# Optimization experiments

Hardware: AMD Instinct MI355X
Metric: run time of the kernel (lower is better)

Reference implementation:

```python
import jax, jax.numpy as jnp
import numpy as np

EPS = 1e-5  # torch LayerNorm default eps
B, N, D_IN, E, H, V = 4096, 32, 256, 128, 512, 32

def _ln(x):
    # LayerNorm without affine (elementwise_affine=False), biased variance
    m = jnp.mean(x, axis=-1, keepdims=True)
    v = jnp.mean(jnp.square(x - m), axis=-1, keepdims=True)
    return (x - m) * jax.lax.rsqrt(v + EPS)

def _ln_gru_cell(x, h, i2h_W, i2h_b, h2h_W, h2h_b, hW_W, hW_b, hU_W, hU_b):
    gates = jax.nn.sigmoid(_ln(x @ i2h_W + i2h_b) + _ln(h @ h2h_W + h2h_b))  # [B,2H]
    hs = h.shape[-1]
    z_t = gates[:, :hs]
    r_t = gates[:, hs:]
    h_hat = jnp.tanh(_ln(x @ hW_W + hW_b) + r_t * _ln(h @ hU_W + hU_b))
    return (1.0 - z_t) * h + z_t * h_hat

def setup_inputs() -> dict:
    key = jax.random.key(0)
    ks = jax.random.split(key, 32)
    std0 = 1.0 / np.sqrt(H)
    u = lambda k, shp: jax.random.uniform(k, shp, jnp.float32, -std0, std0)
    in0 = 3 * E  # attn context + msg embedding + feedback embedding
    inp = {
        'sender_messages_embedded': jax.random.normal(ks[0], (B, E), jnp.float32),
        'prev_hidden': jax.random.normal(ks[1], (2, B, H), jnp.float32),
        'candidate_objects': jax.random.normal(ks[2], (B, N, D_IN), jnp.float32),
        'prev_msg_embedding': jax.random.normal(ks[3], (B, E), jnp.float32),
        # linear_objects_in_keys
        'Wk': jax.random.normal(ks[4], (D_IN, E), jnp.float32) * 0.05,
        'bk': jnp.zeros((E,), jnp.float32),
        # LayerNormGRUCell layer 0 (input 3E)
        'i2h_W0': u(ks[5], (in0, 2 * H)), 'i2h_b0': u(ks[6], (2 * H,)),
        'h2h_W0': u(ks[7], (H, 2 * H)), 'h2h_b0': u(ks[8], (2 * H,)),
        'hW_W0': u(ks[9], (in0, H)), 'hW_b0': u(ks[10], (H,)),
        'hU_W0': u(ks[11], (H, H)), 'hU_b0': u(ks[12], (H,)),
        # LayerNormGRUCell layer 1 (input H)
        'i2h_W1': u(ks[13], (H, 2 * H)), 'i2h_b1': u(ks[14], (2 * H,)),
        'h2h_W1': u(ks[15], (H, 2 * H)), 'h2h_b1': u(ks[16], (2 * H,)),
        'hW_W1': u(ks[17], (H, H)), 'hW_b1': u(ks[18], (H,)),
        'hU_W1': u(ks[19], (H, H)), 'hU_b1': u(ks[20], (H,)),
        # hidden_to_feedback_output
        'out_W': jax.random.normal(ks[21], (H, V), jnp.float32) * 0.05,
        'out_b': jnp.zeros((V,), jnp.float32),
    }
    return inp

def reference(sender_messages_embedded, prev_hidden, candidate_objects, prev_msg_embedding,
              Wk, bk,
              i2h_W0, i2h_b0, h2h_W0, h2h_b0, hW_W0, hW_b0, hU_W0, hU_b0,
              i2h_W1, i2h_b1, h2h_W1, h2h_b1, hW_W1, hW_b1, hU_W1, hU_b1,
              out_W, out_b):
    # object attention (dot): query = msg embedding, keys = projected candidates
    keys = candidate_objects @ Wk + bk                              # [B,N,E]
    scores = jnp.einsum('be,bne->bn', sender_messages_embedded, keys)
    weights = jax.nn.softmax(scores, axis=1)                        # [B,N]
    context = jnp.einsum('bn,bne->be', weights, keys)               # [B,E]
    rnn_input = jnp.concatenate([context, sender_messages_embedded, prev_msg_embedding], axis=-1)  # [B,3E]
    h0 = _ln_gru_cell(rnn_input, prev_hidden[0], i2h_W0, i2h_b0, h2h_W0, h2h_b0, hW_W0, hW_b0, hU_W0, hU_b0)
    h1 = _ln_gru_cell(h0, prev_hidden[1], i2h_W1, i2h_b1, h2h_W1, h2h_b1, hW_W1, hW_b1, hU_W1, hU_b1)
    logits = h1 @ out_W + out_b                                     # [B,V]
    logp = jax.nn.log_softmax(logits, axis=-1)
    probs = jnp.exp(logp)
    entropy = -jnp.sum(probs * logp, axis=-1)                       # [B]
    output_token = jnp.argmax(probs, axis=-1)                       # eval-mode argmax
    output_token_logits = jnp.take_along_axis(logp, output_token[:, None], axis=1)[:, 0]
    new_hidden = jnp.stack([h0, h1])                                # [2,B,H]
    return (output_token, entropy, output_token_logits, logits, new_hidden)
```

## Files before the change

### kernel.cpp

```cpp
#include <hip/hip_runtime.h>
#include <hip/hip_bf16.h>
#include <math.h>

#define B_SZ   4096
#define NCAND  32
#define DIN    256
#define E_SZ   128
#define H_SZ   512
#define VOCAB  32
#define LN_EPS 1e-5f

typedef unsigned short u16;
typedef unsigned int   u32;
typedef __attribute__((ext_vector_type(8))) short  short8;
typedef __attribute__((ext_vector_type(4))) float  floatx4;

static __device__ __forceinline__ float sigmoidf_(float x) {
    return 1.0f / (1.0f + expf(-x));
}
static __device__ __forceinline__ u16 f2bf(float x) {
    u32 u = __float_as_uint(x);
    return (u16)((u + 0x7FFFu + ((u >> 16) & 1u)) >> 16);
}
static __device__ __forceinline__ float bfbits2f(u16 h) {
    return __uint_as_float(((u32)h) << 16);
}

typedef const __attribute__((address_space(1))) unsigned int* gas_ptr;
typedef __attribute__((address_space(3)))       unsigned int* las_ptr;
static __device__ __forceinline__ void gload_lds16(const u16* g, u16* l) {
    __builtin_amdgcn_global_load_lds((gas_ptr)(const void*)g, (las_ptr)(void*)l, 16, 0, 0);
}

static __device__ __forceinline__ void split_store8(const float* __restrict__ g,
                                                    u16* __restrict__ sh,
                                                    u16* __restrict__ sl)
{
    float4 a = *(const float4*)g;
    float4 b = *(const float4*)(g + 4);
    float v[8] = {a.x, a.y, a.z, a.w, b.x, b.y, b.z, b.w};
    union { u16 us[8]; uint4 q; } hb, lb;
    #pragma unroll
    for (int j = 0; j < 8; ++j) {
        u16 h = f2bf(v[j]);
        hb.us[j] = h;
        lb.us[j] = f2bf(v[j] - bfbits2f(h));
    }
    *(uint4*)sh = hb.q;
    *(uint4*)sl = lb.q;
}


__global__ __launch_bounds__(256)
void transpose_split_w(const float* __restrict__ W1, const float* __restrict__ W2,
                       int N1, int N2, int K,
                       u16* __restrict__ Wt_hi, u16* __restrict__ Wt_lo)
{
    __shared__ float t[64][68];
    const int n0 = blockIdx.x * 64, k0 = blockIdx.y * 64;
    const int tid = threadIdx.x;
    const int KT = K >> 5;

    {
        const int kl = tid >> 4, nl4 = (tid & 15) * 4;
        const int ng = n0 + nl4;
        const float* src; int col, ld;
        if (ng < N1) { src = W1; col = ng;      ld = N1; }
        else         { src = W2; col = ng - N1; ld = N2; }
        #pragma unroll
        for (int p = 0; p < 4; ++p) {
            float4 v = *(const float4*)(src + (size_t)(k0 + kl + p * 16) * ld + col);
            *(float4*)&t[kl + p * 16][nl4] = v;
        }
    }
    __syncthreads();

    const int nl = tid >> 2, kc = tid & 3;
    union { u16 us[16]; uint4 v[2]; } hb, lb;
    #pragma unroll
    for (int j = 0; j < 16; ++j) {
        float x = t[kc * 16 + j][nl];
        u16 h = f2bf(x);
        float r = x - bfbits2f(h);
        hb.us[j] = h;
        lb.us[j] = f2bf(r);
    }
    const int n  = n0 + nl;
    const int kb = k0 + kc * 16;
    const size_t off = ((size_t)(n >> 7) * KT + (kb >> 5)) * 4096
                     + (size_t)(n & 127) * 32 + (kb & 31);
    *(uint4*)(Wt_hi + off)     = hb.v[0];
    *(uint4*)(Wt_hi + off + 8) = hb.v[1];
    *(uint4*)(Wt_lo + off)     = lb.v[0];
    *(uint4*)(Wt_lo + off + 8) = lb.v[1];
}

__global__ __launch_bounds__(256)
void bias_cat4_kernel(const float* __restrict__ a0, const float* __restrict__ c0, float* __restrict__ o0,
                      const float* __restrict__ a1, const float* __restrict__ c1, float* __restrict__ o1,
                      const float* __restrict__ a2, const float* __restrict__ c2, float* __restrict__ o2,
                      const float* __restrict__ a3, const float* __restrict__ c3, float* __restrict__ o3)
{
    const int t = blockIdx.x * 256 + threadIdx.x;
    const int w = t / 1536;
    const int i = t - w * 1536;
    const float* a; const float* c; float* o;
    if      (w == 0) { a = a0; c = c0; o = o0; }
    else if (w == 1) { a = a1; c = c1; o = o1; }
    else if (w == 2) { a = a2; c = c2; o = o2; }
    else             { a = a3; c = c3; o = o3; }
    o[i] = (i < 1024) ? a[i] : c[i - 1024];
}

__global__ __launch_bounds__(256)
void split_blocked_kernel(const float* __restrict__ src,
                          u16* __restrict__ hi, u16* __restrict__ lo)
{
    const int i = blockIdx.x * 256 + threadIdx.x;
    const int m = i >> 6, kq = (i & 63) << 3;
    const size_t idx = ((size_t)(m >> 7) * 16 + (kq >> 5)) * 4096
                     + (size_t)(m & 127) * 32 + (kq & 31);
    split_store8(src + (size_t)m * 512 + kq, &hi[idx], &lo[idx]);
}

__global__ __launch_bounds__(256)
void mfma_gemm_dual_kernel(const u16* __restrict__ Axh, const u16* __restrict__ Axl,
                           const u16* __restrict__ Wxh, const u16* __restrict__ Wxl,
                           const float* __restrict__ bx, float* __restrict__ Cx, int KTx,
                           const u16* __restrict__ Ahh, const u16* __restrict__ Ahl,
                           const u16* __restrict__ Whh, const u16* __restrict__ Whl,
                           const float* __restrict__ bh, float* __restrict__ Ch, int KTh)
{
    __shared__ __align__(16) u16 sAh[2][4096];
    __shared__ __align__(16) u16 sAl[2][4096];
    __shared__ __align__(16) u16 sWh[2][4096];
    __shared__ __align__(16) u16 sWl[2][4096];

    const int tid  = threadIdx.x;
    const int lane = tid & 63;
    const int wave = tid >> 6;
    const int wm = (wave >> 1) * 64;
    const int wn = (wave & 1) * 64;
    const int r16 = lane & 15;
    const int q8  = (lane >> 4) * 8;

    const int f   = blockIdx.x;
    const int lin = (f & 7) * 96 + (f >> 3);
    const int sel = lin >= 384;
    const int r   = lin - (sel ? 384 : 0);
    const int mt  = r / 12;
    const int nt  = r - mt * 12;
    const int m_base = mt * 128;
    const int n_base = nt * 128;

    const u16* Ah_  = sel ? Ahh : Axh;
    const u16* Al_  = sel ? Ahl : Axl;
    const u16* Wh_  = sel ? Whh : Wxh;
    const u16* Wl_  = sel ? Whl : Wxl;
    const float* bias = sel ? bh : bx;
    float*       C    = sel ? Ch : Cx;
    const int    KT   = sel ? KTh : KTx;

    const size_t abase = (size_t)(m_base >> 7) * KT * 4096;
    const size_t wbase = (size_t)(n_base >> 7) * KT * 4096;
    const int sofs = wave * 1024;
    const int gofs = sofs + (lane << 3);

    floatx4 acc[4][4] = {};

    {
        const size_t ai = abase + gofs;
        const size_t wi = wbase + gofs;
        gload_lds16(Ah_ + ai,       &sAh[0][sofs]);
        gload_lds16(Ah_ + ai + 512, &sAh[0][sofs + 512]);
        gload_lds16(Al_ + ai,       &sAl[0][sofs]);
        gload_lds16(Al_ + ai + 512, &sAl[0][sofs + 512]);
        gload_lds16(Wh_ + wi,       &sWh[0][sofs]);
        gload_lds16(Wh_ + wi + 512, &sWh[0][sofs + 512]);
        gload_lds16(Wl_ + wi,       &sWl[0][sofs]);
        gload_lds16(Wl_ + wi + 512, &sWl[0][sofs + 512]);
    }

    int cur = 0;
    for (int kt = 0; kt < KT; ++kt) {
        __syncthreads();

        const int nxt = cur ^ 1;
        if (kt + 1 < KT) {
            const size_t ai = abase + (size_t)(kt + 1) * 4096 + gofs;
            const size_t wi = wbase + (size_t)(kt + 1) * 4096 + gofs;
            gload_lds16(Ah_ + ai,       &sAh[nxt][sofs]);
            gload_lds16(Ah_ + ai + 512, &sAh[nxt][sofs + 512]);
            gload_lds16(Al_ + ai,       &sAl[nxt][sofs]);
            gload_lds16(Al_ + ai + 512, &sAl[nxt][sofs + 512]);
            gload_lds16(Wh_ + wi,       &sWh[nxt][sofs]);
            gload_lds16(Wh_ + wi + 512, &sWh[nxt][sofs + 512]);
            gload_lds16(Wl_ + wi,       &sWl[nxt][sofs]);
            gload_lds16(Wl_ + wi + 512, &sWl[nxt][sofs + 512]);
        }

        short8 ah[4], al[4], bhf[4], blf[4];
        #pragma unroll
        for (int i = 0; i < 4; ++i) {
            const int ar = (wm + i * 16 + r16) * 32 + q8;
            ah[i] = *(const short8*)&sAh[cur][ar];
            al[i] = *(const short8*)&sAl[cur][ar];
            const int br = (wn + i * 16 + r16) * 32 + q8;
            bhf[i] = *(const short8*)&sWh[cur][br];
            blf[i] = *(const short8*)&sWl[cur][br];
        }
        #pragma unroll
        for (int i = 0; i < 4; ++i)
            #pragma unroll
            for (int j = 0; j < 4; ++j) {
                acc[i][j] = __builtin_amdgcn_mfma_f32_16x16x32_bf16(ah[i], bhf[j], acc[i][j], 0, 0, 0);
                acc[i][j] = __builtin_amdgcn_mfma_f32_16x16x32_bf16(ah[i], blf[j], acc[i][j], 0, 0, 0);
                acc[i][j] = __builtin_amdgcn_mfma_f32_16x16x32_bf16(al[i], bhf[j], acc[i][j], 0, 0, 0);
            }

        cur = nxt;
    }

    const int quad = lane >> 4;
    #pragma unroll
    for (int j = 0; j < 4; ++j) {
        const int n = n_base + wn + j * 16 + r16;
        const float bv = bias[n];
        #pragma unroll
        for (int i = 0; i < 4; ++i) {
            #pragma unroll
            for (int rr = 0; rr < 4; ++rr) {
                const int m = m_base + wm + i * 16 + quad * 4 + rr;
                C[(size_t)m * 1536 + n] = acc[i][j][rr] + bv;
            }
        }
    }
}

__global__ __launch_bounds__(256)
void gemm_bt64_kernel(const float* __restrict__ A, const float* __restrict__ Bt,
                      float* __restrict__ C, int M, int N, int K, int ldc)
{
    __shared__ float As[16][68];
    __shared__ float Bs[16][68];

    const int tid = threadIdx.x;
    const int bm = blockIdx.y * 64;
    const int bn = blockIdx.x * 64;
    const int tx = tid & 15, ty = tid >> 4;
    const int m0 = ty * 4, n0 = tx * 4;
    const int arow = tid >> 2, acol = (tid & 3) * 4;

    float acc[4][4] = {};

    for (int k0 = 0; k0 < K; k0 += 16) {
        float4 a4 = *(const float4*)(A  + (size_t)(bm + arow) * K + (k0 + acol));
        float4 b4 = *(const float4*)(Bt + (size_t)(bn + arow) * K + (k0 + acol));
        As[acol + 0][arow] = a4.x; As[acol + 1][arow] = a4.y;
        As[acol + 2][arow] = a4.z; As[acol + 3][arow] = a4.w;
        Bs[acol + 0][arow] = b4.x; Bs[acol + 1][arow] = b4.y;
        Bs[acol + 2][arow] = b4.z; Bs[acol + 3][arow] = b4.w;
        __syncthreads();
        #pragma unroll
        for (int k = 0; k < 16; ++k) {
            float4 av = *(const float4*)&As[k][m0];
            float4 bv = *(const float4*)&Bs[k][n0];
            float aa[4] = {av.x, av.y, av.z, av.w};
            float bb[4] = {bv.x, bv.y, bv.z, bv.w};
            #pragma unroll
            for (int i = 0; i < 4; ++i)
                #pragma unroll
                for (int j = 0; j < 4; ++j)
                    acc[i][j] = fmaf(aa[i], bb[j], acc[i][j]);
        }
        __syncthreads();
    }

    #pragma unroll
    for (int i = 0; i < 4; ++i)
        *(float4*)(C + (size_t)(bm + m0 + i) * ldc + bn + n0) =
            make_float4(acc[i][0], acc[i][1], acc[i][2], acc[i][3]);
}

__global__ __launch_bounds__(256)
void attn_ctx_kernel(const float* __restrict__ co, const float* __restrict__ q,
                     const float* __restrict__ snd, const float* __restrict__ pmsg,
                     float* __restrict__ cbar,
                     u16* __restrict__ rinh, u16* __restrict__ rinl)
{
    __shared__ float s_q[DIN];
    __shared__ float s_scores[NCAND];
    __shared__ float s_w[NCAND];

    const int b   = blockIdx.x;
    const int tid = threadIdx.x;
    const float* cob = co + (size_t)b * NCAND * DIN;

    if (tid < DIN) s_q[tid] = q[(size_t)b * DIN + tid];
    __syncthreads();

    {
        const int n = tid >> 3, part = tid & 7;
        const float* con = cob + n * DIN;
        float sc = 0.f;
        #pragma unroll
        for (int qq = 0; qq < 8; ++qq) {
            const int d = part * 4 + qq * 32;
            float4 cv = *(const float4*)(con + d);
            float4 qv = *(const float4*)&s_q[d];
            sc += cv.x * qv.x + cv.y * qv.y + cv.z * qv.z + cv.w * qv.w;
        }
        #pragma unroll
        for (int m = 4; m; m >>= 1) sc += __shfl_xor(sc, m);
        if (part == 0) s_scores[n] = sc;
    }
    __syncthreads();

    if (tid < NCAND) {
        float s  = s_scores[tid];
        float mx = s;
        #pragma unroll
        for (int m = 16; m; m >>= 1) mx = fmaxf(mx, __shfl_xor(mx, m));
        float e = expf(s - mx);
        float sum = e;
        #pragma unroll
        for (int m = 16; m; m >>= 1) sum += __shfl_xor(sum, m);
        s_w[tid] = e / sum;
    }
    __syncthreads();

    {
        float cb = 0.f;
        #pragma unroll
        for (int n = 0; n < NCAND; ++n) cb = fmaf(s_w[n], cob[n * DIN + tid], cb);
        cbar[(size_t)b * DIN + tid] = cb;
    }
    {
        const float x = (tid < 128) ? snd[(size_t)b * E_SZ + tid]
                                    : pmsg[(size_t)b * E_SZ + (tid - 128)];
        const int d = 128 + tid;
        const u16 h = f2bf(x);
        const u16 l = f2bf(x - bfbits2f(h));
        const size_t idx = ((size_t)(b >> 7) * 12 + (d >> 5)) * 4096
                         + (size_t)(b & 127) * 32 + (d & 31);
        rinh[idx] = h;
        rinl[idx] = l;
    }
}

__global__ __launch_bounds__(256)
void gemm_ctx_kernel(const float* __restrict__ A, const float* __restrict__ Bm,
                     const float* __restrict__ bias,
                     u16* __restrict__ rinh, u16* __restrict__ rinl)
{
    __shared__ float As[16][68];
    __shared__ float Bs[16][68];

    const int tid = threadIdx.x;
    const int bm = blockIdx.y * 64;
    const int bn = blockIdx.x * 64;
    const int tx = tid & 15, ty = tid >> 4;
    const int m0 = ty * 4, n0 = tx * 4;
    const int arow = tid >> 2, acol = (tid & 3) * 4;
    const int brow = tid >> 4, bcol = (tid & 15) * 4;
    const int K = 256, N = 128;

    float acc[4][4] = {};

    for (int k0 = 0; k0 < K; k0 += 16) {
        float4 a4 = *(const float4*)(A + (size_t)(bm + arow) * K + (k0 + acol));
        float4 b4 = *(const float4*)(Bm + (size_t)(k0 + brow) * N + (bn + bcol));
        As[acol + 0][arow] = a4.x; As[acol + 1][arow] = a4.y;
        As[acol + 2][arow] = a4.z; As[acol + 3][arow] = a4.w;
        *(float4*)&Bs[brow][bcol] = b4;
        __syncthreads();
        #pragma unroll
        for (int k = 0; k < 16; ++k) {
            float4 av = *(const float4*)&As[k][m0];
            float4 bv = *(const float4*)&Bs[k][n0];
            float aa[4] = {av.x, av.y, av.z, av.w};
            float bb[4] = {bv.x, bv.y, bv.z, bv.w};
            #pragma unroll
            for (int i = 0; i < 4; ++i)
                #pragma unroll
                for (int j = 0; j < 4; ++j)
                    acc[i][j] = fmaf(aa[i], bb[j], acc[i][j]);
        }
        __syncthreads();
    }

    const float4 bv = *(const float4*)(bias + bn + n0);
    #pragma unroll
    for (int i = 0; i < 4; ++i) {
        float o0 = acc[i][0] + bv.x, o1 = acc[i][1] + bv.y;
        float o2 = acc[i][2] + bv.z, o3 = acc[i][3] + bv.w;
        const int m = bm + m0 + i;
        const int d = bn + n0;
        const u16 h0 = f2bf(o0), h1 = f2bf(o1), h2 = f2bf(o2), h3 = f2bf(o3);
        const u16 l0 = f2bf(o0 - bfbits2f(h0));
        const u16 l1 = f2bf(o1 - bfbits2f(h1));
        const u16 l2 = f2bf(o2 - bfbits2f(h2));
        const u16 l3 = f2bf(o3 - bfbits2f(h3));
        const size_t idx = ((size_t)(m >> 7) * 12 + (d >> 5)) * 4096
                         + (size_t)(m & 127) * 32 + (d & 31);
        uint2 hv, lv;
        hv.x = (u32)h0 | ((u32)h1 << 16); hv.y = (u32)h2 | ((u32)h3 << 16);
        lv.x = (u32)l0 | ((u32)l1 << 16); lv.y = (u32)l2 | ((u32)l3 << 16);
        *(uint2*)&rinh[idx] = hv;
        *(uint2*)&rinl[idx] = lv;
    }
}

__global__ __launch_bounds__(256)
void gru_combine_kernel(const float* __restrict__ gxc, const float* __restrict__ ghc,
                        const float* __restrict__ hprev, float* __restrict__ hout,
                        u16* __restrict__ himg_hi, u16* __restrict__ himg_lo)
{
    const int b    = blockIdx.x;
    const int tid  = threadIdx.x;
    const int lane = tid & 63, wv = tid >> 6;

    __shared__ float s_part[4][8];
    __shared__ float s_gates[1024];

    const float* gxb = gxc + (size_t)b * 1536;
    const float* ghb = ghc + (size_t)b * 1536;

    const float4 gx4 = *(const float4*)(gxb + tid * 4);
    const float4 gh4 = *(const float4*)(ghb + tid * 4);
    const float2 cx2 = *(const float2*)(gxb + 1024 + tid * 2);
    const float2 ch2 = *(const float2*)(ghb + 1024 + tid * 2);

    float v[8];
    v[0] = gx4.x + gx4.y + gx4.z + gx4.w;
    v[1] = gx4.x*gx4.x + gx4.y*gx4.y + gx4.z*gx4.z + gx4.w*gx4.w;
    v[2] = gh4.x + gh4.y + gh4.z + gh4.w;
    v[3] = gh4.x*gh4.x + gh4.y*gh4.y + gh4.z*gh4.z + gh4.w*gh4.w;
    v[4] = cx2.x + cx2.y;
    v[5] = cx2.x*cx2.x + cx2.y*cx2.y;
    v[6] = ch2.x + ch2.y;
    v[7] = ch2.x*ch2.x + ch2.y*ch2.y;

    #pragma unroll
    for (int i = 0; i < 8; ++i)
        #pragma unroll
        for (int m = 32; m; m >>= 1) v[i] += __shfl_xor(v[i], m);

    if (lane == 0) {
        #pragma unroll
        for (int i = 0; i < 8; ++i) s_part[wv][i] = v[i];
    }
    __syncthreads();

    float t[8];
    #pragma unroll
    for (int i = 0; i < 8; ++i)
        t[i] = s_part[0][i] + s_part[1][i] + s_part[2][i] + s_part[3][i];

    const float mgx = t[0] / 1024.f;
    const float rgx = 1.f / sqrtf(t[1] / 1024.f - mgx * mgx + LN_EPS);
    const float mgh = t[2] / 1024.f;
    const float rgh = 1.f / sqrtf(t[3] / 1024.f - mgh * mgh + LN_EPS);
    const float mcx = t[4] / 512.f;
    const float rcx = 1.f / sqrtf(t[5] / 512.f - mcx * mcx + LN_EPS);
    const float mch = t[6] / 512.f;
    const float rch = 1.f / sqrtf(t[7] / 512.f - mch * mch + LN_EPS);

    float4 g;
    g.x = sigmoidf_((gx4.x - mgx) * rgx + (gh4.x - mgh) * rgh);
    g.y = sigmoidf_((gx4.y - mgx) * rgx + (gh4.y - mgh) * rgh);
    g.z = sigmoidf_((gx4.z - mgx) * rgx + (gh4.z - mgh) * rgh);
    g.w = sigmoidf_((gx4.w - mgx) * rgx + (gh4.w - mgh) * rgh);
    *(float4*)&s_gates[tid * 4] = g;
    __syncthreads();

    const float2 hp2 = *(const float2*)(hprev + (size_t)b * 512 + tid * 2);
    const float z0 = s_gates[tid * 2 + 0];
    const float z1 = s_gates[tid * 2 + 1];
    const float r0 = s_gates[512 + tid * 2 + 0];
    const float r1 = s_gates[512 + tid * 2 + 1];

    const float hh0 = tanhf((cx2.x - mcx) * rcx + r0 * ((ch2.x - mch) * rch));
    const float hh1 = tanhf((cx2.y - mcx) * rcx + r1 * ((ch2.y - mch) * rch));
    const float hn0 = (1.f - z0) * hp2.x + z0 * hh0;
    const float hn1 = (1.f - z1) * hp2.y + z1 * hh1;

    *(float2*)(hout + (size_t)b * 512 + tid * 2) = make_float2(hn0, hn1);

    if (himg_hi) {
        const u16 h0b = f2bf(hn0), h1b = f2bf(hn1);
        const u16 l0b = f2bf(hn0 - bfbits2f(h0b));
        const u16 l1b = f2bf(hn1 - bfbits2f(h1b));
        const int k = tid * 2;
        const size_t idx = ((size_t)(b >> 7) * 16 + (k >> 5)) * 4096
                         + (size_t)(b & 127) * 32 + (k & 31);
        *(u32*)&himg_hi[idx] = (u32)h0b | ((u32)h1b << 16);
        *(u32*)&himg_lo[idx] = (u32)l0b | ((u32)l1b << 16);
    }
}

__global__ __launch_bounds__(256)
void out_kernel(const float* __restrict__ h1, const float* __restrict__ W,
                const float* __restrict__ bias, float* __restrict__ out)
{
    __shared__ float s_h[4][512];
    const int wave = threadIdx.x >> 6, lane = threadIdx.x & 63;
    const int b = blockIdx.x * 4 + wave;

    {
        const float4* hp = (const float4*)(h1 + (size_t)b * 512);
        float4* sp = (float4*)&s_h[wave][0];
        sp[lane]      = hp[lane];
        sp[lane + 64] = hp[lane + 64];
    }
    __syncthreads();

    const int v = lane & 31, half = lane >> 5;
    float acc = 0.f;
    {
        const float* wp = W + (size_t)half * 256 * 32 + v;
        const float* hh = &s_h[wave][half * 256];
        for (int k = 0; k < 256; ++k) acc = fmaf(hh[k], wp[(size_t)k * 32], acc);
    }
    acc += __shfl_xor(acc, 32);
    const float logit = acc + bias[v];

    if (half == 0)
        out[(size_t)3 * B_SZ + (size_t)b * VOCAB + v] = logit;

    float mval = logit; int midx = v;
    #pragma unroll
    for (int m = 16; m; m >>= 1) {
        float ov = __shfl_xor(mval, m);
        int   oi = __shfl_xor(midx, m);
        if (ov > mval || (ov == mval && oi < midx)) { mval = ov; midx = oi; }
    }
    float ex = expf(logit - mval);
    float sum = ex;
    #pragma unroll
    for (int m = 16; m; m >>= 1) sum += __shfl_xor(sum, m);
    const float lse  = mval + logf(sum);
    const float logp = logit - lse;
    const float p    = expf(logp);
    float epl = p * logp;
    #pragma unroll
    for (int m = 16; m; m >>= 1) epl += __shfl_xor(epl, m);
    const float entropy = -epl;
    const float tok_logp = __shfl(logp, midx, 32);

    if (lane == 0) {
        out[b]             = (float)midx;
        out[B_SZ + b]      = entropy;
        out[2 * B_SZ + b]  = tok_logp;
    }
}

extern "C" void kernel_launch(void* const* d_in, const int* in_sizes, int n_in,
                              void* d_out, int out_size, void* d_ws, size_t ws_size,
                              hipStream_t stream)
{
    const float* snd    = (const float*)d_in[0];
    const float* ph     = (const float*)d_in[1];
    const float* co     = (const float*)d_in[2];
    const float* pmsg   = (const float*)d_in[3];
    const float* Wk     = (const float*)d_in[4];
    const float* bk     = (const float*)d_in[5];
    const float* i2hW0  = (const float*)d_in[6];
    const float* i2hb0  = (const float*)d_in[7];
    const float* h2hW0  = (const float*)d_in[8];
    const float* h2hb0  = (const float*)d_in[9];
    const float* hWW0   = (const float*)d_in[10];
    const float* hWb0   = (const float*)d_in[11];
    const float* hUW0   = (const float*)d_in[12];
    const float* hUb0   = (const float*)d_in[13];
    const float* i2hW1  = (const float*)d_in[14];
    const float* i2hb1  = (const float*)d_in[15];
    const float* h2hW1  = (const float*)d_in[16];
    const float* h2hb1  = (const float*)d_in[17];
    const float* hWW1   = (const float*)d_in[18];
    const float* hWb1   = (const float*)d_in[19];
    const float* hUW1   = (const float*)d_in[20];
    const float* hUb1   = (const float*)d_in[21];
    const float* outW   = (const float*)d_in[22];
    const float* outb   = (const float*)d_in[23];

    float* out = (float*)d_out;
    float* h0out = out + (size_t)3 * B_SZ + (size_t)B_SZ * VOCAB;
    float* h1out = h0out + (size_t)B_SZ * H_SZ;

    const float* h0prev = ph;
    const float* h1prev = ph + (size_t)B_SZ * H_SZ;

    char* p = (char*)d_ws;
    auto alloc_f = [&](size_t n) { float* r = (float*)p; p += n * 4; return r; };
    auto alloc_h = [&](size_t n) { u16* r = (u16*)p; p += ((n * 2 + 15) & ~15ull); return r; };

    float* qbuf   = alloc_f((size_t)B_SZ * 256);
    float* cbar   = alloc_f((size_t)B_SZ * 256);
    float* gxc    = alloc_f((size_t)B_SZ * 1536);
    float* ghc    = alloc_f((size_t)B_SZ * 1536);
    u16* rin_hi = alloc_h((size_t)B_SZ * 384);
    u16* rin_lo = alloc_h((size_t)B_SZ * 384);
    u16* php_hi = alloc_h((size_t)2 * B_SZ * 512);
    u16* php_lo = alloc_h((size_t)2 * B_SZ * 512);
    u16* h0i_hi = alloc_h((size_t)B_SZ * 512);
    u16* h0i_lo = alloc_h((size_t)B_SZ * 512);
    u16* W0x_hi = alloc_h((size_t)1536 * 384);
    u16* W0x_lo = alloc_h((size_t)1536 * 384);
    u16* W0h_hi = alloc_h((size_t)1536 * 512);
    u16* W0h_lo = alloc_h((size_t)1536 * 512);
    u16* W1x_hi = alloc_h((size_t)1536 * 512);
    u16* W1x_lo = alloc_h((size_t)1536 * 512);
    u16* W1h_hi = alloc_h((size_t)1536 * 512);
    u16* W1h_lo = alloc_h((size_t)1536 * 512);
    float* b0x = alloc_f(1536);
    float* b0h = alloc_f(1536);
    float* b1x = alloc_f(1536);
    float* b1h = alloc_f(1536);

    transpose_split_w<<<dim3(24, 6), 256, 0, stream>>>(i2hW0, hWW0, 1024, 512, 384, W0x_hi, W0x_lo);
    transpose_split_w<<<dim3(24, 8), 256, 0, stream>>>(h2hW0, hUW0, 1024, 512, 512, W0h_hi, W0h_lo);
    transpose_split_w<<<dim3(24, 8), 256, 0, stream>>>(i2hW1, hWW1, 1024, 512, 512, W1x_hi, W1x_lo);
    transpose_split_w<<<dim3(24, 8), 256, 0, stream>>>(h2hW1, hUW1, 1024, 512, 512, W1h_hi, W1h_lo);
    bias_cat4_kernel<<<24, 256, 0, stream>>>(i2hb0, hWb0, b0x, h2hb0, hUb0, b0h,
                                             i2hb1, hWb1, b1x, h2hb1, hUb1, b1h);
    split_blocked_kernel<<<2 * B_SZ * 64 / 256, 256, 0, stream>>>(ph, php_hi, php_lo);

    gemm_bt64_kernel<<<dim3(4, 64), 256, 0, stream>>>(snd, Wk, qbuf, B_SZ, 256, 128, 256);
    attn_ctx_kernel<<<B_SZ, 256, 0, stream>>>(co, qbuf, snd, pmsg, cbar, rin_hi, rin_lo);
    gemm_ctx_kernel<<<dim3(2, 64), 256, 0, stream>>>(cbar, Wk, bk, rin_hi, rin_lo);

    mfma_gemm_dual_kernel<<<768, 256, 0, stream>>>(
        rin_hi, rin_lo, W0x_hi, W0x_lo, b0x, gxc, 12,
        php_hi, php_lo, W0h_hi, W0h_lo, b0h, ghc, 16);
    gru_combine_kernel<<<B_SZ, 256, 0, stream>>>(gxc, ghc, h0prev, h0out, h0i_hi, h0i_lo);

    mfma_gemm_dual_kernel<<<768, 256, 0, stream>>>(
        h0i_hi, h0i_lo, W1x_hi, W1x_lo, b1x, gxc, 16,
        php_hi + (size_t)B_SZ * 512, php_lo + (size_t)B_SZ * 512,
        W1h_hi, W1h_lo, b1h, ghc, 16);
    gru_combine_kernel<<<B_SZ, 256, 0, stream>>>(gxc, ghc, h1prev, h1out, (u16*)nullptr, (u16*)nullptr);

    out_kernel<<<B_SZ / 4, 256, 0, stream>>>(h1out, outW, outb, out);
}
```

Baseline: 441.3 us.

## Load A fragments directly from global into registers, staging only W through LDS

The dual GEMM kernel no longer stages the A operand (hi/lo bf16 splits) in shared memory. Each wave reads its A fragments straight from global into registers, using a ping-pong register set while the loop is unrolled by two K-tiles. W tiles are still double-buffered in LDS through async global-to-LDS loads. This halves LDS footprint and LDS traffic, but adds register pressure and relies on A rows in each wave being read without cross-wave reuse; the unroll-by-two assumes KT is even.

```diff
diff --git a/kernel.cpp b/kernel.cpp
--- a/kernel.cpp
+++ b/kernel.cpp
@@ -131,8 +131,6 @@
                            const u16* __restrict__ Whh, const u16* __restrict__ Whl,
                            const float* __restrict__ bh, float* __restrict__ Ch, int KTh)
 {
-    __shared__ __align__(16) u16 sAh[2][4096];
-    __shared__ __align__(16) u16 sAl[2][4096];
     __shared__ __align__(16) u16 sWh[2][4096];
     __shared__ __align__(16) u16 sWl[2][4096];
 
@@ -161,64 +159,102 @@
     float*       C    = sel ? Ch : Cx;
     const int    KT   = sel ? KTh : KTx;
 
-    const size_t abase = (size_t)(m_base >> 7) * KT * 4096;
+    const u16* Ah0 = Ah_ + (size_t)(m_base >> 7) * KT * 4096;
+    const u16* Al0 = Al_ + (size_t)(m_base >> 7) * KT * 4096;
     const size_t wbase = (size_t)(n_base >> 7) * KT * 4096;
     const int sofs = wave * 1024;
     const int gofs = sofs + (lane << 3);
 
+    int aoff[4];
+    #pragma unroll
+    for (int i = 0; i < 4; ++i) aoff[i] = (wm + i * 16 + r16) * 32 + q8;
+
+    int boff[4];
+    #pragma unroll
+    for (int i = 0; i < 4; ++i) boff[i] = (wn + i * 16 + r16) * 32 + q8;
+
     floatx4 acc[4][4] = {};
 
+    short8 aAh[4], aAl[4];
+    short8 aBh[4], aBl[4];
+
     {
-        const size_t ai = abase + gofs;
         const size_t wi = wbase + gofs;
-        gload_lds16(Ah_ + ai,       &sAh[0][sofs]);
-        gload_lds16(Ah_ + ai + 512, &sAh[0][sofs + 512]);
-        gload_lds16(Al_ + ai,       &sAl[0][sofs]);
-        gload_lds16(Al_ + ai + 512, &sAl[0][sofs + 512]);
         gload_lds16(Wh_ + wi,       &sWh[0][sofs]);
         gload_lds16(Wh_ + wi + 512, &sWh[0][sofs + 512]);
         gload_lds16(Wl_ + wi,       &sWl[0][sofs]);
         gload_lds16(Wl_ + wi + 512, &sWl[0][sofs + 512]);
-    }
-
-    int cur = 0;
-    for (int kt = 0; kt < KT; ++kt) {
+        #pragma unroll
+        for (int i = 0; i < 4; ++i) {
+            aAh[i] = *(const short8*)(Ah0 + aoff[i]);
+            aAl[i] = *(const short8*)(Al0 + aoff[i]);
+        }
+    }
+
+    for (int kt = 0; kt < KT; kt += 2) {
         __syncthreads();
 
-        const int nxt = cur ^ 1;
-        if (kt + 1 < KT) {
-            const size_t ai = abase + (size_t)(kt + 1) * 4096 + gofs;
+        {
             const size_t wi = wbase + (size_t)(kt + 1) * 4096 + gofs;
-            gload_lds16(Ah_ + ai,       &sAh[nxt][sofs]);
-            gload_lds16(Ah_ + ai + 512, &sAh[nxt][sofs + 512]);
-            gload_lds16(Al_ + ai,       &sAl[nxt][sofs]);
-            gload_lds16(Al_ + ai + 512, &sAl[nxt][sofs + 512]);
-            gload_lds16(Wh_ + wi,       &sWh[nxt][sofs]);
-            gload_lds16(Wh_ + wi + 512, &sWh[nxt][sofs + 512]);
-            gload_lds16(Wl_ + wi,       &sWl[nxt][sofs]);
-            gload_lds16(Wl_ + wi + 512, &sWl[nxt][sofs + 512]);
-        }
-
-        short8 ah[4], al[4], bhf[4], blf[4];
-        #pragma unroll
-        for (int i = 0; i < 4; ++i) {
-            const int ar = (wm + i * 16 + r16) * 32 + q8;
-            ah[i] = *(const short8*)&sAh[cur][ar];
-            al[i] = *(const short8*)&sAl[cur][ar];
-            const int br = (wn + i * 16 + r16) * 32 + q8;
-            bhf[i] = *(const short8*)&sWh[cur][br];
-            blf[i] = *(const short8*)&sWl[cur][br];
-        }
-        #pragma unroll
-        for (int i = 0; i < 4; ++i)
-            #pragma unroll
-            for (int j = 0; j < 4; ++j) {
-                acc[i][j] = __builtin_amdgcn_mfma_f32_16x16x32_bf16(ah[i], bhf[j], acc[i][j], 0, 0, 0);
-                acc[i][j] = __builtin_amdgcn_mfma_f32_16x16x32_bf16(ah[i], blf[j], acc[i][j], 0, 0, 0);
-                acc[i][j] = __builtin_amdgcn_mfma_f32_16x16x32_bf16(al[i], bhf[j], acc[i][j], 0, 0, 0);
+            gload_lds16(Wh_ + wi,       &sWh[1][sofs]);
+            gload_lds16(Wh_ + wi + 512, &sWh[1][sofs + 512]);
+            gload_lds16(Wl_ + wi,       &sWl[1][sofs]);
+            gload_lds16(Wl_ + wi + 512, &sWl[1][sofs + 512]);
+            const size_t ai = (size_t)(kt + 1) * 4096;
+            #pragma unroll
+            for (int i = 0; i < 4; ++i) {
+                aBh[i] = *(const short8*)(Ah0 + ai + aoff[i]);
+                aBl[i] = *(const short8*)(Al0 + ai + aoff[i]);
             }
-
-        cur = nxt;
+        }
+        {
+            short8 bhf[4], blf[4];
+            #pragma unroll
+            for (int i = 0; i < 4; ++i) {
+                bhf[i] = *(const short8*)&sWh[0][boff[i]];
+                blf[i] = *(const short8*)&sWl[0][boff[i]];
+            }
+            #pragma unroll
+            for (int i = 0; i < 4; ++i)
+                #pragma unroll
+                for (int j = 0; j < 4; ++j) {
+                    acc[i][j] = __builtin_amdgcn_mfma_f32_16x16x32_bf16(aAh[i], bhf[j], acc[i][j], 0, 0, 0);
+                    acc[i][j] = __builtin_amdgcn_mfma_f32_16x16x32_bf16(aAh[i], blf[j], acc[i][j], 0, 0, 0);
+                    acc[i][j] = __builtin_amdgcn_mfma_f32_16x16x32_bf16(aAl[i], bhf[j], acc[i][j], 0, 0, 0);
+                }
+        }
+
+        __syncthreads();
+
+        if (kt + 2 < KT) {
+            const size_t wi = wbase + (size_t)(kt + 2) * 4096 + gofs;
+            gload_lds16(Wh_ + wi,       &sWh[0][sofs]);
+            gload_lds16(Wh_ + wi + 512, &sWh[0][sofs + 512]);
+            gload_lds16(Wl_ + wi,       &sWl[0][sofs]);
+            gload_lds16(Wl_ + wi + 512, &sWl[0][sofs + 512]);
+            const size_t ai = (size_t)(kt + 2) * 4096;
+            #pragma unroll
+            for (int i = 0; i < 4; ++i) {
+                aAh[i] = *(const short8*)(Ah0 + ai + aoff[i]);
+                aAl[i] = *(const short8*)(Al0 + ai + aoff[i]);
+            }
+        }
+        {
+            short8 bhf[4], blf[4];
+            #pragma unroll
+            for (int i = 0; i < 4; ++i) {
+                bhf[i] = *(const short8*)&sWh[1][boff[i]];
+                blf[i] = *(const short8*)&sWl[1][boff[i]];
+            }
+            #pragma unroll
+            for (int i = 0; i < 4; ++i)
+                #pragma unroll
+                for (int j = 0; j < 4; ++j) {
+                    acc[i][j] = __builtin_amdgcn_mfma_f32_16x16x32_bf16(aBh[i], bhf[j], acc[i][j], 0, 0, 0);
+                    acc[i][j] = __builtin_amdgcn_mfma_f32_16x16x32_bf16(aBh[i], blf[j], acc[i][j], 0, 0, 0);
+                    acc[i][j] = __builtin_amdgcn_mfma_f32_16x16x32_bf16(aBl[i], bhf[j], acc[i][j], 0, 0, 0);
+                }
+        }
     }
 
     const int quad = lane >> 4;
```

Measured after the change: 462.4 us. 4.8% more time.
